# Performance work log

Hardware: AMD Instinct MI355X
Metric: run time of the kernel (lower is better)

## Reference

```python
import jax, jax.numpy as jnp
import numpy as np

N_PER_GROUP = 64
INPUT_DIM = 512
BATCH = 16384


def setup_inputs() -> dict:
    key = jax.random.key(0)
    k1, k2, k3 = jax.random.split(key, 3)
    x = jax.random.normal(k1, (BATCH, INPUT_DIM), dtype=jnp.float32)
    # xavier-uniform-ish prototypes
    prototype_vectors = jax.random.normal(k2, (2, N_PER_GROUP, INPUT_DIM), dtype=jnp.float32) * 0.05
    # mixture_fn = Linear(2*d, d)
    W_mix = jax.random.normal(k3, (INPUT_DIM, 2 * INPUT_DIM), dtype=jnp.float32) * (1.0 / np.sqrt(2 * INPUT_DIM))
    b_mix = jnp.zeros((INPUT_DIM,), dtype=jnp.float32)
    return {"x": x, "prototype_vectors": prototype_vectors, "W_mix": W_mix, "b_mix": b_mix}


def _mixed_prototypes(prototype_vectors, W_mix, b_mix):
    # Batched replacement of the nested j,l Python loop:
    # pair (j,l) -> concat(proto[0,j], proto[1,l]) -> Linear(2d -> d)
    n, d = prototype_vectors.shape[1], prototype_vectors.shape[2]
    g0 = jnp.broadcast_to(prototype_vectors[0][:, None, :], (n, n, d))  # [j,l,d]
    g1 = jnp.broadcast_to(prototype_vectors[1][None, :, :], (n, n, d))  # [j,l,d]
    pairs = jnp.concatenate([g0, g1], axis=-1).reshape(n * n, 2 * d)     # [n^2, 2d]
    return pairs @ W_mix.T + b_mix                                       # [n^2, d]


def reference(x, prototype_vectors, W_mix, b_mix):
    p = _mixed_prototypes(prototype_vectors, W_mix, b_mix)  # [P, d]
    # list_of_distances: pairwise squared Euclidean distance [B, P]
    xx = jnp.sum(x * x, axis=-1, keepdims=True)         # [B,1]
    pp = jnp.sum(p * p, axis=-1)[None, :]               # [1,P]
    return xx - 2.0 * (x @ p.T) + pp                    # [B,P]
```

## Files before the change

### kernel.cpp

```cpp
#include <hip/hip_runtime.h>
#include <hip/hip_bf16.h>

#define BATCH 16384
#define DIM   512
#define NPG   64
#define NPAIR 4096
#define NA    128

typedef float f32x4 __attribute__((ext_vector_type(4)));
typedef short s16x8 __attribute__((ext_vector_type(8)));
typedef unsigned short u16;

static __device__ __forceinline__ u16 f2bf(float f) {
    union { float f; unsigned u; } v; v.f = f;
    unsigned r = (v.u + 0x7FFFu + ((v.u >> 16) & 1u)) >> 16;
    return (u16)r;
}

__global__ __launch_bounds__(256) void kA_mixA(const float* __restrict__ proto,
                                               const float* __restrict__ W,
                                               float* __restrict__ Af,
                                               u16* __restrict__ Ab) {
    int gid = blockIdx.x * 256 + threadIdx.x;
    int h = gid & 1;
    int j = (gid >> 1) & 127;
    int d = gid >> 8;
    int koff = (j < NPG ? 0 : DIM) + h * (DIM / 2);
    const float4* pr = (const float4*)(proto + j * DIM + h * (DIM / 2));
    const float4* wr = (const float4*)(W + d * (2 * DIM) + koff);
    float a0 = 0.f, a1 = 0.f, a2 = 0.f, a3 = 0.f;
#pragma unroll 4
    for (int k4 = 0; k4 < DIM / 8; ++k4) {
        float4 p = pr[k4], w = wr[k4];
        a0 += p.x * w.x; a1 += p.y * w.y; a2 += p.z * w.z; a3 += p.w * w.w;
    }
    float a = (a0 + a1) + (a2 + a3);
    a += __shfl_xor(a, 1);
    if (h == 0) {
        Af[j * DIM + d] = a;
        Ab[j * DIM + d] = f2bf(a);
    }
}

__global__ __launch_bounds__(256) void k2_pp(const float* __restrict__ Af,
                                             const float* __restrict__ bm,
                                             float* __restrict__ pp) {
    int wave = (blockIdx.x * blockDim.x + threadIdx.x) >> 6;
    int lane = threadIdx.x & 63;
    int j = wave >> 6, l = wave & 63;
    const float4* r0 = (const float4*)(Af + j * DIM);
    const float4* r1 = (const float4*)(Af + (NPG + l) * DIM);
    const float4* bb = (const float4*)bm;
    float acc = 0.f;
#pragma unroll
    for (int i = 0; i < 2; ++i) {
        int idx = lane * 2 + i;
        float4 v0 = r0[idx], v1 = r1[idx], vb = bb[idx];
        float s;
        s = v0.x + v1.x + vb.x; acc += s * s;
        s = v0.y + v1.y + vb.y; acc += s * s;
        s = v0.z + v1.z + vb.z; acc += s * s;
        s = v0.w + v1.w + vb.w; acc += s * s;
    }
#pragma unroll
    for (int off = 32; off > 0; off >>= 1) acc += __shfl_xor(acc, off);
    if (lane == 0) pp[wave] = acc;
}

__global__ __launch_bounds__(512) void kFD(const float* __restrict__ x,
                                           const u16* __restrict__ Ab,
                                           const float* __restrict__ bm,
                                           const float* __restrict__ pp,
                                           float* __restrict__ out) {
    __shared__ u16   xsb[16 * 512];
    __shared__ float Ut[16][NA];
    __shared__ float xxs[16], ws2[16];
    __shared__ float rbl[16];
    int t = threadIdx.x;
    int lane = t & 63;
    int w = t >> 6;
    int m0 = blockIdx.x * 16;

    {
        int row = t >> 5;
        int c0 = (t & 31) * 4;
        const float* xrow = x + (size_t)(m0 + row) * DIM;
        float xx = 0.f, wdot = 0.f;
#pragma unroll
        for (int i = 0; i < 4; ++i) {
            int col = c0 + i * 128;
            float4 v = *(const float4*)(xrow + col);
            float4 b = *(const float4*)(bm + col);
            xx   += v.x * v.x + v.y * v.y + v.z * v.z + v.w * v.w;
            wdot += v.x * b.x + v.y * b.y + v.z * b.z + v.w * b.w;
            ushort4 hv;
            hv.x = f2bf(v.x); hv.y = f2bf(v.y); hv.z = f2bf(v.z); hv.w = f2bf(v.w);
            int byte = (row * 1024 + col * 2) ^ ((row & 7) << 4);
            *(ushort4*)((char*)xsb + byte) = hv;
        }
#pragma unroll
        for (int off = 16; off > 0; off >>= 1) {
            xx   += __shfl_xor(xx, off);
            wdot += __shfl_xor(wdot, off);
        }
        if ((t & 31) == 0) { xxs[row] = xx; ws2[row] = wdot; }
    }
    __syncthreads();
    if (t < 16) rbl[t] = xxs[t] - 2.0f * ws2[t];

    {
        int r = lane & 15, g = lane >> 4;
        int ct = w;
        f32x4 acc = (f32x4){0.f, 0.f, 0.f, 0.f};
        const u16* brow = Ab + (size_t)(ct * 16 + r) * DIM;
#pragma unroll
        for (int k0 = 0; k0 < 16; ++k0) {
            int byte = (r * 1024 + k0 * 64 + g * 16) ^ ((r & 7) << 4);
            s16x8 af = *(const s16x8*)((const char*)xsb + byte);
            s16x8 bf = *(const s16x8*)(brow + k0 * 32 + g * 8);
            acc = __builtin_amdgcn_mfma_f32_16x16x32_bf16(af, bf, acc, 0, 0, 0);
        }
#pragma unroll
        for (int rr = 0; rr < 4; ++rr)
            Ut[g * 4 + rr][ct * 16 + r] = acc[rr];
    }
    __syncthreads();

    {
        int l4 = (lane & 15) * 4;
#pragma unroll
        for (int rl = 0; rl < 2; ++rl) {
            int row = w * 2 + rl;
            float base0 = rbl[row];
            const float* Ur = Ut[row];
            float4 v4 = *(const float4*)(Ur + NPG + l4);
            float c0 = -2.0f * v4.x, c1 = -2.0f * v4.y;
            float c2 = -2.0f * v4.z, c3 = -2.0f * v4.w;
            float* orow = out + (size_t)(m0 + row) * NPAIR;
#pragma unroll
            for (int i = 0; i < 16; ++i) {
                int idx = (i * 64 + lane) * 4;
                int j = idx >> 6;
                float s = base0 - 2.0f * Ur[j];
                float4 p4 = *(const float4*)(pp + idx);
                float4 o;
                o.x = s + p4.x + c0;
                o.y = s + p4.y + c1;
                o.z = s + p4.z + c2;
                o.w = s + p4.w + c3;
                *(float4*)(orow + idx) = o;
            }
        }
    }
}

extern "C" void kernel_launch(void* const* d_in, const int* in_sizes, int n_in,
                              void* d_out, int out_size, void* d_ws, size_t ws_size,
                              hipStream_t stream) {
    const float* x     = (const float*)d_in[0];
    const float* proto = (const float*)d_in[1];
    const float* Wmix  = (const float*)d_in[2];
    const float* bmix  = (const float*)d_in[3];
    float* out = (float*)d_out;

    float* ws = (float*)d_ws;
    float* Af = ws;
    float* pp = ws + 65536;
    u16*   Ab = (u16*)(ws + 65536 + 4096);

    kA_mixA<<<512, 256, 0, stream>>>(proto, Wmix, Af, Ab);
    k2_pp  <<<1024, 256, 0, stream>>>(Af, bmix, pp);
    kFD    <<<1024, 512, 0, stream>>>(x, Ab, bmix, pp, out);
}
```

Before: 92.69 us.

## Process two 16-row x tiles per block with both tiles' loads issued upfront

The fused distance kernel now handles 32 batch rows per block in two 16-row stages, with double-buffered shared memory for the bf16 x tile and the U projections. All global x loads for both stages are issued at kernel start, so the second tile's load latency is hidden behind the first tile's MFMA and output writes. The grid shrinks to half as many blocks, which amortises the per-block bias load but roughly doubles shared memory use and register pressure. Fewer blocks may also reduce the latency hiding that comes from running many blocks concurrently.

After: 99.84 us. 1.08x slower.

```diff
diff --git a/kernel.cpp b/kernel.cpp
--- a/kernel.cpp
+++ b/kernel.cpp
@@ -67,90 +67,105 @@
     if (lane == 0) pp[wave] = acc;
 }
 
-__global__ __launch_bounds__(512) void kFD(const float* __restrict__ x,
+__global__ __launch_bounds__(512) void kFE(const float* __restrict__ x,
                                            const u16* __restrict__ Ab,
                                            const float* __restrict__ bm,
                                            const float* __restrict__ pp,
                                            float* __restrict__ out) {
-    __shared__ u16   xsb[16 * 512];
-    __shared__ float Ut[16][NA];
-    __shared__ float xxs[16], ws2[16];
-    __shared__ float rbl[16];
+    __shared__ u16   xsb[2][16 * 512];
+    __shared__ float Ut[2][16][NA];
+    __shared__ float xxs[2][16], ws2[2][16];
+    __shared__ float rbl[2][16];
     int t = threadIdx.x;
     int lane = t & 63;
     int w = t >> 6;
-    int m0 = blockIdx.x * 16;
+    int m0 = blockIdx.x * 32;
 
+    int row = t >> 5;
+    int c0 = (t & 31) * 4;
+    int r = lane & 15, g = lane >> 4;
+
+    float4 bmv[4], v0[4], v1[4];
     {
-        int row = t >> 5;
-        int c0 = (t & 31) * 4;
-        const float* xrow = x + (size_t)(m0 + row) * DIM;
-        float xx = 0.f, wdot = 0.f;
+        const float* xr0 = x + (size_t)(m0 + row) * DIM;
+        const float* xr1 = x + (size_t)(m0 + 16 + row) * DIM;
 #pragma unroll
         for (int i = 0; i < 4; ++i) {
-            int col = c0 + i * 128;
-            float4 v = *(const float4*)(xrow + col);
-            float4 b = *(const float4*)(bm + col);
-            xx   += v.x * v.x + v.y * v.y + v.z * v.z + v.w * v.w;
-            wdot += v.x * b.x + v.y * b.y + v.z * b.z + v.w * b.w;
-            ushort4 hv;
-            hv.x = f2bf(v.x); hv.y = f2bf(v.y); hv.z = f2bf(v.z); hv.w = f2bf(v.w);
-            int byte = (row * 1024 + col * 2) ^ ((row & 7) << 4);
-            *(ushort4*)((char*)xsb + byte) = hv;
+            bmv[i] = *(const float4*)(bm + c0 + i * 128);
+            v0[i]  = *(const float4*)(xr0 + c0 + i * 128);
+            v1[i]  = *(const float4*)(xr1 + c0 + i * 128);
         }
+    }
+
 #pragma unroll
-        for (int off = 16; off > 0; off >>= 1) {
-            xx   += __shfl_xor(xx, off);
-            wdot += __shfl_xor(wdot, off);
+    for (int s = 0; s < 2; ++s) {
+        {
+            float xx = 0.f, wdot = 0.f;
+#pragma unroll
+            for (int i = 0; i < 4; ++i) {
+                float4 v = (s == 0) ? v0[i] : v1[i];
+                float4 b = bmv[i];
+                int col = c0 + i * 128;
+                xx   += v.x * v.x + v.y * v.y + v.z * v.z + v.w * v.w;
+                wdot += v.x * b.x + v.y * b.y + v.z * b.z + v.w * b.w;
+                ushort4 hv;
+                hv.x = f2bf(v.x); hv.y = f2bf(v.y); hv.z = f2bf(v.z); hv.w = f2bf(v.w);
+                int byte = (row * 1024 + col * 2) ^ ((row & 7) << 4);
+                *(ushort4*)((char*)xsb[s] + byte) = hv;
+            }
+#pragma unroll
+            for (int off = 16; off > 0; off >>= 1) {
+                xx   += __shfl_xor(xx, off);
+                wdot += __shfl_xor(wdot, off);
+            }
+            if ((t & 31) == 0) { xxs[s][row] = xx; ws2[s][row] = wdot; }
         }
-        if ((t & 31) == 0) { xxs[row] = xx; ws2[row] = wdot; }
-    }
-    __syncthreads();
-    if (t < 16) rbl[t] = xxs[t] - 2.0f * ws2[t];
+        __syncthreads();
+        if (t < 16) rbl[s][t] = xxs[s][t] - 2.0f * ws2[s][t];
 
-    {
-        int r = lane & 15, g = lane >> 4;
-        int ct = w;
-        f32x4 acc = (f32x4){0.f, 0.f, 0.f, 0.f};
-        const u16* brow = Ab + (size_t)(ct * 16 + r) * DIM;
+        {
+            f32x4 acc = (f32x4){0.f, 0.f, 0.f, 0.f};
+            const u16* brow = Ab + (size_t)(w * 16 + r) * DIM;
 #pragma unroll
-        for (int k0 = 0; k0 < 16; ++k0) {
-            int byte = (r * 1024 + k0 * 64 + g * 16) ^ ((r & 7) << 4);
-            s16x8 af = *(const s16x8*)((const char*)xsb + byte);
-            s16x8 bf = *(const s16x8*)(brow + k0 * 32 + g * 8);
-            acc = __builtin_amdgcn_mfma_f32_16x16x32_bf16(af, bf, acc, 0, 0, 0);
+            for (int k0 = 0; k0 < 16; ++k0) {
+                int byte = (r * 1024 + k0 * 64 + g * 16) ^ ((r & 7) << 4);
+                s16x8 af = *(const s16x8*)((const char*)xsb[s] + byte);
+                s16x8 bf = *(const s16x8*)(brow + k0 * 32 + g * 8);
+                acc = __builtin_amdgcn_mfma_f32_16x16x32_bf16(af, bf, acc, 0, 0, 0);
+            }
+#pragma unroll
+            for (int rr = 0; rr < 4; ++rr)
+                Ut[s][g * 4 + rr][w * 16 + r] = acc[rr];
         }
+        __syncthreads();
+
+        {
+            int l4 = (lane & 15) * 4;
 #pragma unroll
-        for (int rr = 0; rr < 4; ++rr)
-            Ut[g * 4 + rr][ct * 16 + r] = acc[rr];
-    }
-    __syncthreads();
-
-    {
-        int l4 = (lane & 15) * 4;
+            for (int rl = 0; rl < 2; ++rl) {
+                int rw = w * 2 + rl;
+                float base0 = rbl[s][rw];
+                const float* Ur = Ut[s][rw];
+                float4 v4 = *(const float4*)(Ur + NPG + l4);
+                float cc0 = -2.0f * v4.x, cc1 = -2.0f * v4.y;
+                float cc2 = -2.0f * v4.z, cc3 = -2.0f * v4.w;
+                float* orow = out + (size_t)(m0 + s * 16 + rw) * NPAIR;
 #pragma unroll
-        for (int rl = 0; rl < 2; ++rl) {
-            int row = w * 2 + rl;
-            float base0 = rbl[row];
-            const float* Ur = Ut[row];
-            float4 v4 = *(const float4*)(Ur + NPG + l4);
-            float c0 = -2.0f * v4.x, c1 = -2.0f * v4.y;
-            float c2 = -2.0f * v4.z, c3 = -2.0f * v4.w;
-            float* orow = out + (size_t)(m0 + row) * NPAIR;
-#pragma unroll
-            for (int i = 0; i < 16; ++i) {
-                int idx = (i * 64 + lane) * 4;
-                int j = idx >> 6;
-                float s = base0 - 2.0f * Ur[j];
-                float4 p4 = *(const float4*)(pp + idx);
-                float4 o;
-                o.x = s + p4.x + c0;
-                o.y = s + p4.y + c1;
-                o.z = s + p4.z + c2;
-                o.w = s + p4.w + c3;
-                *(float4*)(orow + idx) = o;
+                for (int i = 0; i < 16; ++i) {
+                    int idx = (i * 64 + lane) * 4;
+                    int j = idx >> 6;
+                    float sv = base0 - 2.0f * Ur[j];
+                    float4 p4 = *(const float4*)(pp + idx);
+                    float4 o;
+                    o.x = sv + p4.x + cc0;
+                    o.y = sv + p4.y + cc1;
+                    o.z = sv + p4.z + cc2;
+                    o.w = sv + p4.w + cc3;
+                    *(float4*)(orow + idx) = o;
+                }
             }
         }
+        if (s == 0) __syncthreads();
     }
 }
 
@@ -170,5 +185,5 @@
 
     kA_mixA<<<512, 256, 0, stream>>>(proto, Wmix, Af, Ab);
     k2_pp  <<<1024, 256, 0, stream>>>(Af, bmix, pp);
-    kFD    <<<1024, 512, 0, stream>>>(x, Ab, bmix, pp, out);
+    kFE    <<<512, 512, 0, stream>>>(x, Ab, bmix, pp, out);
 }
```
